# Optimization experiments

Measured on AMD Instinct MI355X. Metric: run time of the kernel, lower is better.

Reference implementation:

```python
import jax, jax.numpy as jnp
import numpy as np

N, E = 100000, 1600000
IN, EDGE_DIM, HID, OUT, HEADS = 128, 16, 32, 32, 2


def _glorot(key, shape, scale=0.1):
    return jax.random.normal(key, shape, dtype=jnp.float32) * scale


def setup_inputs() -> dict:
    key = jax.random.key(0)
    ks = jax.random.split(key, 20)
    HC1 = HEADS * HID
    return {
        "x": jax.random.normal(ks[0], (N, IN), dtype=jnp.float32),
        "edge_index": jax.random.randint(ks[1], (2, E), 0, N, dtype=jnp.int32),
        "edge_attr": jax.random.normal(ks[2], (E, EDGE_DIM), dtype=jnp.float32),
        # layer 1 (heads=HEADS, concat=True)
        "W1l": _glorot(ks[3], (IN, HC1)), "b1l": jnp.zeros((HC1,), jnp.float32),
        "W1r": _glorot(ks[4], (IN, HC1)), "b1r": jnp.zeros((HC1,), jnp.float32),
        "W1e": _glorot(ks[5], (EDGE_DIM, HC1)),
        "att1": _glorot(ks[6], (HEADS, HID)),
        "bias1": jnp.zeros((HC1,), jnp.float32),
        # layer 2 (heads=1, concat=False)
        "W2l": _glorot(ks[7], (HC1, HID)), "b2l": jnp.zeros((HID,), jnp.float32),
        "W2r": _glorot(ks[8], (HC1, HID)), "b2r": jnp.zeros((HID,), jnp.float32),
        "W2e": _glorot(ks[9], (EDGE_DIM, HID)),
        "att2": _glorot(ks[10], (1, HID)),
        "bias2": jnp.zeros((HID,), jnp.float32),
        # final linear
        "Wlin": _glorot(ks[11], (HID, OUT)), "blin": jnp.zeros((OUT,), jnp.float32),
    }


def gatv2_layer(x, src, dst, edge_attr, Wl, bl, Wr, br, We, att, bias, H, C, concat):
    n = x.shape[0]
    xl = (x @ Wl + bl).reshape(n, H, C)   # source transform (lin_l)
    xr = (x @ Wr + br).reshape(n, H, C)   # target transform (lin_r)
    ea = (edge_attr @ We).reshape(-1, H, C)
    m = xl[src] + xr[dst] + ea                       # [E, H, C]
    e = jnp.sum(jax.nn.leaky_relu(m, 0.2) * att, axis=-1)  # [E, H]
    # segment softmax over incoming edges of each destination node
    emax = jax.ops.segment_max(e, dst, num_segments=n)
    emax = jnp.where(jnp.isfinite(emax), emax, 0.0)
    ee = jnp.exp(e - emax[dst])
    denom = jax.ops.segment_sum(ee, dst, num_segments=n)
    alpha = ee / (denom[dst] + 1e-16)                # [E, H]
    out = jax.ops.segment_sum(xl[src] * alpha[..., None], dst, num_segments=n)  # [N, H, C]
    out = out.reshape(n, H * C) if concat else out.mean(axis=1)
    return out + bias


def reference(x, edge_index, edge_attr, W1l, b1l, W1r, b1r, W1e, att1, bias1,
              W2l, b2l, W2r, b2r, W2e, att2, bias2, Wlin, blin):
    src, dst = edge_index[0], edge_index[1]
    h = jax.nn.elu(gatv2_layer(x, src, dst, edge_attr, W1l, b1l, W1r, b1r, W1e,
                               att1, bias1, HEADS, HID, True))
    h = jax.nn.elu(gatv2_layer(h, src, dst, edge_attr, W2l, b2l, W2r, b2r, W2e,
                               att2, bias2, 1, HID, False))
    return h @ Wlin + blin
```

## Files before the change

### kernel.cpp

```cpp
#include <hip/hip_runtime.h>
#include <hip/hip_fp16.h>
#include <cstdint>
#include <cstddef>


typedef _Float16 half8 __attribute__((ext_vector_type(8)));
typedef float f32x4 __attribute__((ext_vector_type(4)));

__global__ void hist_kernel(const int* __restrict__ dst, int* __restrict__ deg, int E) {
    int e = blockIdx.x * blockDim.x + threadIdx.x;
    if (e < E) atomicAdd(&deg[dst[e]], 1);
}

__global__ void scan_part(const int* __restrict__ deg, int* __restrict__ bsum, int n) {
    int tid = threadIdx.x;
    int base = blockIdx.x * 1024 + tid * 4;
    int s = 0;
#pragma unroll
    for (int j = 0; j < 4; ++j) {
        int i = base + j;
        if (i < n) s += deg[i];
    }
#pragma unroll
    for (int off = 1; off < 64; off <<= 1) s += __shfl_xor(s, off, 64);
    __shared__ int ws[4];
    if ((tid & 63) == 0) ws[tid >> 6] = s;
    __syncthreads();
    if (tid == 0) bsum[blockIdx.x] = ws[0] + ws[1] + ws[2] + ws[3];
}

__global__ void scan_mid(int* __restrict__ bsum, int* __restrict__ rowstart, int nb, int n) {
    int tid = threadIdx.x;
    int v = (tid < nb) ? bsum[tid] : 0;
    int incl = v;
#pragma unroll
    for (int off = 1; off < 64; off <<= 1) {
        int t = __shfl_up(incl, off, 64);
        if ((tid & 63) >= off) incl += t;
    }
    __shared__ int w0;
    if (tid == 63) w0 = incl;
    __syncthreads();
    if (tid >= 64) incl += w0;
    if (tid < nb) bsum[tid] = incl - v;
    if (tid == nb - 1) rowstart[n] = incl;
}

__global__ void scan_fin(const int* __restrict__ deg, const int* __restrict__ bsum,
                         int* __restrict__ rowstart, int n) {
    int tid = threadIdx.x;
    int lane = tid & 63, wid = tid >> 6;
    int base = blockIdx.x * 1024 + tid * 4;
    int v[4];
    int s = 0;
#pragma unroll
    for (int j = 0; j < 4; ++j) {
        int i = base + j;
        v[j] = (i < n) ? deg[i] : 0;
        s += v[j];
    }
    int incl = s;
#pragma unroll
    for (int off = 1; off < 64; off <<= 1) {
        int t = __shfl_up(incl, off, 64);
        if (lane >= off) incl += t;
    }
    __shared__ int ws[4];
    if (lane == 63) ws[wid] = incl;
    __syncthreads();
    int wofs = 0;
    for (int w2 = 0; w2 < wid; ++w2) wofs += ws[w2];
    int acc = bsum[blockIdx.x] + wofs + (incl - s);
#pragma unroll
    for (int j = 0; j < 4; ++j) {
        int i = base + j;
        if (i < n) rowstart[i] = acc;
        acc += v[j];
    }
}

__global__ void scatter_kernel(const int* __restrict__ src, const int* __restrict__ dst,
                               const float* __restrict__ eattr,
                               const int* __restrict__ rowstart, int* __restrict__ cursor,
                               int* __restrict__ src_sorted, __half* __restrict__ eah_sorted,
                               int E) {
    int e = blockIdx.x * blockDim.x + threadIdx.x;
    if (e < E) {
        int d = dst[e];
        int p = atomicAdd(&cursor[d], 1);
        int pos = rowstart[d] + p;
        src_sorted[pos] = src[e];
        const float4* s4 = (const float4*)&eattr[(size_t)e * 16];
        float4 a = s4[0], b = s4[1], c = s4[2], f = s4[3];
        __half2 h[8];
        h[0] = __float22half2_rn(make_float2(a.x, a.y));
        h[1] = __float22half2_rn(make_float2(a.z, a.w));
        h[2] = __float22half2_rn(make_float2(b.x, b.y));
        h[3] = __float22half2_rn(make_float2(b.z, b.w));
        h[4] = __float22half2_rn(make_float2(c.x, c.y));
        h[5] = __float22half2_rn(make_float2(c.z, c.w));
        h[6] = __float22half2_rn(make_float2(f.x, f.y));
        h[7] = __float22half2_rn(make_float2(f.z, f.w));
        int4* o = (int4*)&eah_sorted[(size_t)pos * 16];
        o[0] = *(int4*)&h[0];
        o[1] = *(int4*)&h[4];
    }
}

template <int K, int Mh>
__global__ void wprep_kernel(const float* __restrict__ Wl, const float* __restrict__ Wr,
                             __half* __restrict__ Wfrag) {
    constexpr int KS = K / 32;
    constexpr int BN = 2 * Mh;
    int i = blockIdx.x * blockDim.x + threadIdx.x;
    if (i >= K * BN) return;
    int j = i & 7;
    int lane = (i >> 3) & 63;
    int rest = i >> 9;
    int ks = rest % KS;
    int nt = rest / KS;
    int k = ks * 32 + ((lane >> 4) & 3) * 8 + j;
    int col = nt * 16 + (lane & 15);
    float v = (col < Mh) ? Wl[k * Mh + col] : Wr[k * Mh + (col - Mh)];
    Wfrag[i] = __float2half(v);
}

template <int K, int Mh, int BM>
__global__ __launch_bounds__(256) void gemm_mfma(
    const float* __restrict__ x, const __half* __restrict__ Wfrag,
    const float* __restrict__ bl, const float* __restrict__ br,
    __half* __restrict__ yl, __half* __restrict__ yr, int n) {
    constexpr int BN = 2 * Mh;
    constexpr int KS = K / 32;
    constexpr int NT = BN / 16;
    constexpr int RW = BM / 64;
    constexpr int LDP = K + 8;
    __shared__ __half xs[BM * LDP];
    int tid = threadIdx.x;
    int lane = tid & 63;
    int wave = tid >> 6;
    int node0 = blockIdx.x * BM;
    constexpr int ITER = (BM * K) / (256 * 4);
#pragma unroll
    for (int it = 0; it < ITER; ++it) {
        int base = (it * 256 + tid) * 4;
        int row = base / K, kk = base % K;
        float4 v = make_float4(0.f, 0.f, 0.f, 0.f);
        if (node0 + row < n) v = *(const float4*)&x[(size_t)(node0 + row) * K + kk];
        __half2* d = (__half2*)&xs[row * LDP + kk];
        d[0] = __float22half2_rn(make_float2(v.x, v.y));
        d[1] = __float22half2_rn(make_float2(v.z, v.w));
    }
    __syncthreads();
    f32x4 acc[RW][NT];
#pragma unroll
    for (int r = 0; r < RW; ++r)
#pragma unroll
        for (int t = 0; t < NT; ++t) {
            f32x4 z = {0.f, 0.f, 0.f, 0.f};
            acc[r][t] = z;
        }
    int r0 = lane & 15, kof = (lane >> 4) * 8;
#pragma unroll
    for (int ks = 0; ks < KS; ++ks) {
        half8 a[RW];
#pragma unroll
        for (int r = 0; r < RW; ++r) {
            int row = (wave * RW + r) * 16 + r0;
            a[r] = *reinterpret_cast<const half8*>(&xs[row * LDP + ks * 32 + kof]);
        }
#pragma unroll
        for (int t = 0; t < NT; ++t) {
            half8 b = *reinterpret_cast<const half8*>(&Wfrag[(((size_t)t * KS + ks) * 64 + lane) * 8]);
#pragma unroll
            for (int r = 0; r < RW; ++r)
                acc[r][t] = __builtin_amdgcn_mfma_f32_16x16x32_f16(a[r], b, acc[r][t], 0, 0, 0);
        }
    }
#pragma unroll
    for (int r = 0; r < RW; ++r) {
#pragma unroll
        for (int t = 0; t < NT; ++t) {
            int col = t * 16 + (lane & 15);
            float bv = (col < Mh) ? bl[col] : br[col - Mh];
#pragma unroll
            for (int q = 0; q < 4; ++q) {
                int node = node0 + (wave * RW + r) * 16 + (lane >> 4) * 4 + q;
                if (node < n) {
                    float v = acc[r][t][q] + bv;
                    if (col < Mh) yl[(size_t)node * Mh + col] = __float2half(v);
                    else          yr[(size_t)node * Mh + (col - Mh)] = __float2half(v);
                }
            }
        }
    }
}

template <int K, int M, int NPB>
__global__ void linear_kernel(const float* __restrict__ x, const float* __restrict__ W,
                              const float* __restrict__ b, float* __restrict__ y, int n) {
    __shared__ float sx[NPB * K];
    int tid = threadIdx.x;
    int node0 = blockIdx.x * NPB;
    for (int i = tid; i < NPB * K; i += NPB * M) {
        int nn = node0 + i / K;
        sx[i] = (nn < n) ? x[(size_t)nn * K + (i % K)] : 0.f;
    }
    __syncthreads();
    int ln = tid / M, m = tid % M;
    int node = node0 + ln;
    if (node >= n) return;
    float acc = b[m];
#pragma unroll
    for (int k = 0; k < K; ++k) acc = fmaf(sx[ln * K + k], W[k * M + m], acc);
    y[(size_t)node * M + m] = acc;
}

template <int H, int C>
__global__ __launch_bounds__(256) void fused_edge_agg(
    const int* __restrict__ rowstart, const int* __restrict__ src_sorted,
    const __half* __restrict__ eah_sorted,
    const float* __restrict__ We,
    const float* __restrict__ att,
    const __half* __restrict__ xl, const __half* __restrict__ xr,
    const float* __restrict__ bias, float* __restrict__ out, int n) {
    constexpr int HC = H * C;
    constexpr int LPN = HC / 2;
    constexpr int NPW = 64 / LPN;
    int gt = blockIdx.x * blockDim.x + threadIdx.x;
    int wave = gt >> 6;
    int lane = threadIdx.x & 63;
    int sub = lane / LPN;
    int j = lane % LPN;
    int ch0 = 2 * j;
    int node = wave * NPW + sub;
    if (node >= n) return;
    __half2 wh[16];
#pragma unroll
    for (int k = 0; k < 16; ++k) wh[k] = __float22half2_rn(*(const float2*)&We[k * HC + ch0]);
    float2 a2 = *(const float2*)&att[ch0];
    float2 xr2 = __half22float2(*(const __half2*)&xr[(size_t)node * HC + ch0]);
    int beg = rowstart[node], end = rowstart[node + 1];
    float denom = 0.f, acc0 = 0.f, acc1 = 0.f;

    auto gemv = [&](const float4& r0, const float4& r1, const __half2& xlh,
                    float& m0, float& m1, float2& xlf) {
        const __half2* h0 = (const __half2*)&r0;
        const __half2* h1 = (const __half2*)&r1;
        __half2 p0 = __hmul2(__low2half2(h0[0]), wh[0]);
        __half2 p1 = __hmul2(__high2half2(h0[0]), wh[1]);
        p0 = __hfma2(__low2half2(h0[1]), wh[2], p0);
        p1 = __hfma2(__high2half2(h0[1]), wh[3], p1);
        p0 = __hfma2(__low2half2(h0[2]), wh[4], p0);
        p1 = __hfma2(__high2half2(h0[2]), wh[5], p1);
        p0 = __hfma2(__low2half2(h0[3]), wh[6], p0);
        p1 = __hfma2(__high2half2(h0[3]), wh[7], p1);
        p0 = __hfma2(__low2half2(h1[0]), wh[8], p0);
        p1 = __hfma2(__high2half2(h1[0]), wh[9], p1);
        p0 = __hfma2(__low2half2(h1[1]), wh[10], p0);
        p1 = __hfma2(__high2half2(h1[1]), wh[11], p1);
        p0 = __hfma2(__low2half2(h1[2]), wh[12], p0);
        p1 = __hfma2(__high2half2(h1[2]), wh[13], p1);
        p0 = __hfma2(__low2half2(h1[3]), wh[14], p0);
        p1 = __hfma2(__high2half2(h1[3]), wh[15], p1);
        float2 mf = __half22float2(__hadd2(p0, p1));
        xlf = __half22float2(xlh);
        m0 = xlf.x + xr2.x + mf.x;
        m1 = xlf.y + xr2.y + mf.y;
    };
    auto logit = [&](float m0, float m1) -> float {
        m0 = (m0 > 0.f) ? m0 : 0.2f * m0;
        m1 = (m1 > 0.f) ? m1 : 0.2f * m1;
        float v = m0 * a2.x + m1 * a2.y;
#pragma unroll
        for (int msk = 1; msk < 16; msk <<= 1) v += __shfl_xor(v, msk, 64);
        return v;
    };

    int pp = beg;
    for (; pp + 2 <= end; pp += 2) {
        int s0 = src_sorted[pp];
        int s1 = src_sorted[pp + 1];
        const float4* qa = (const float4*)&eah_sorted[(size_t)pp * 16];
        const float4* qb = (const float4*)&eah_sorted[((size_t)pp + 1) * 16];
        float4 r0a = qa[0], r1a = qa[1];
        float4 r0b = qb[0], r1b = qb[1];
        __half2 xh0 = *(const __half2*)&xl[(size_t)s0 * HC + ch0];
        __half2 xh1 = *(const __half2*)&xl[(size_t)s1 * HC + ch0];
        float m0a, m1a, m0b, m1b;
        float2 xla, xlb;
        gemv(r0a, r1a, xh0, m0a, m1a, xla);
        gemv(r0b, r1b, xh1, m0b, m1b, xlb);
        float wa = __expf(logit(m0a, m1a));
        float wb = __expf(logit(m0b, m1b));
        denom += wa + wb;
        acc0 = fmaf(xla.x, wa, acc0);
        acc1 = fmaf(xla.y, wa, acc1);
        acc0 = fmaf(xlb.x, wb, acc0);
        acc1 = fmaf(xlb.y, wb, acc1);
    }
    if (pp < end) {
        int s0 = src_sorted[pp];
        const float4* qa = (const float4*)&eah_sorted[(size_t)pp * 16];
        float4 r0a = qa[0], r1a = qa[1];
        __half2 xh0 = *(const __half2*)&xl[(size_t)s0 * HC + ch0];
        float m0a, m1a;
        float2 xla;
        gemv(r0a, r1a, xh0, m0a, m1a, xla);
        float wa = __expf(logit(m0a, m1a));
        denom += wa;
        acc0 = fmaf(xla.x, wa, acc0);
        acc1 = fmaf(xla.y, wa, acc1);
    }
    float2 b2 = *(const float2*)&bias[ch0];
    float inv = 1.f / (denom + 1e-16f);
    float o0 = acc0 * inv + b2.x;
    float o1 = acc1 * inv + b2.y;
    o0 = (o0 > 0.f) ? o0 : __expf(o0) - 1.f;
    o1 = (o1 > 0.f) ? o1 : __expf(o1) - 1.f;
    *(float2*)&out[(size_t)node * HC + ch0] = make_float2(o0, o1);
}

extern "C" void kernel_launch(void* const* d_in, const int* in_sizes, int n_in,
                              void* d_out, int out_size, void* d_ws, size_t ws_size,
                              hipStream_t stream) {
    const float* x     = (const float*)d_in[0];
    const int*   eidx  = (const int*)d_in[1];
    const float* eattr = (const float*)d_in[2];
    const float* W1l   = (const float*)d_in[3];
    const float* b1l   = (const float*)d_in[4];
    const float* W1r   = (const float*)d_in[5];
    const float* b1r   = (const float*)d_in[6];
    const float* W1e   = (const float*)d_in[7];
    const float* att1  = (const float*)d_in[8];
    const float* bias1 = (const float*)d_in[9];
    const float* W2l   = (const float*)d_in[10];
    const float* b2l   = (const float*)d_in[11];
    const float* W2r   = (const float*)d_in[12];
    const float* b2r   = (const float*)d_in[13];
    const float* W2e   = (const float*)d_in[14];
    const float* att2  = (const float*)d_in[15];
    const float* bias2 = (const float*)d_in[16];
    const float* Wlin  = (const float*)d_in[17];
    const float* blin  = (const float*)d_in[18];

    const int N = in_sizes[0] / 128;
    const int E = in_sizes[1] / 2;
    const int* src = eidx;
    const int* dst = eidx + E;

    char* p = (char*)d_ws;
    auto take = [&](size_t bytes) {
        char* r = p;
        p += (bytes + 255) & ~(size_t)255;
        return r;
    };
    int*    deg        = (int*)take((size_t)N * sizeof(int));
    int*    cursor     = (int*)take((size_t)N * sizeof(int));
    int*    rowstart   = (int*)take((size_t)(N + 1) * sizeof(int));
    int*    bsum       = (int*)take(256 * sizeof(int));
    int*    src_sorted = (int*)take((size_t)E * sizeof(int));
    __half* eah_sorted = (__half*)take((size_t)E * 16 * sizeof(__half));
    __half* A          = (__half*)take((size_t)N * 64 * sizeof(__half));
    __half* B          = (__half*)take((size_t)N * 64 * sizeof(__half));
    float*  Cbuf       = (float*)take((size_t)N * 64 * sizeof(float));
    __half* Wf1        = (__half*)take((size_t)128 * 128 * sizeof(__half));
    __half* Wf2        = (__half*)take((size_t)64 * 64 * sizeof(__half));

    (void)hipMemsetAsync(deg, 0, (size_t)N * sizeof(int), stream);
    (void)hipMemsetAsync(cursor, 0, (size_t)N * sizeof(int), stream);
    hist_kernel<<<(E + 255) / 256, 256, 0, stream>>>(dst, deg, E);
    {
        int nb = (N + 1023) / 1024;
        scan_part<<<nb, 256, 0, stream>>>(deg, bsum, N);
        scan_mid<<<1, 128, 0, stream>>>(bsum, rowstart, nb, N);
        scan_fin<<<nb, 256, 0, stream>>>(deg, bsum, rowstart, N);
    }
    scatter_kernel<<<(E + 255) / 256, 256, 0, stream>>>(src, dst, eattr, rowstart, cursor,
                                                        src_sorted, eah_sorted, E);
    wprep_kernel<128, 64><<<(128 * 128 + 255) / 256, 256, 0, stream>>>(W1l, W1r, Wf1);
    wprep_kernel<64, 32><<<(64 * 64 + 255) / 256, 256, 0, stream>>>(W2l, W2r, Wf2);

    gemm_mfma<128, 64, 64><<<(N + 63) / 64, 256, 0, stream>>>(x, Wf1, b1l, b1r, A, B, N);
    fused_edge_agg<2, 32><<<(int)(((size_t)((N + 1) / 2) * 64 + 255) / 256), 256, 0, stream>>>(
        rowstart, src_sorted, eah_sorted, W1e, att1, A, B, bias1, Cbuf, N);

    gemm_mfma<64, 32, 128><<<(N + 127) / 128, 256, 0, stream>>>(Cbuf, Wf2, b2l, b2r, A, B, N);
    fused_edge_agg<1, 32><<<(int)(((size_t)((N + 3) / 4) * 64 + 255) / 256), 256, 0, stream>>>(
        rowstart, src_sorted, eah_sorted, W2e, att2, A, B, bias2, Cbuf, N);

    linear_kernel<32, 32, 8><<<(N + 7) / 8, 256, 0, stream>>>(Cbuf, Wlin, blin, (float*)d_out, N);
}
```

Baseline: 457.9 us.

## Sort nodes by degree and keep edge attributes in original order

Adds a degree-bucketed node permutation so each wave processes nodes of similar in-degree, which reduces intra-wave divergence in the edge loop. The scatter now writes fp16 edge attributes in original edge order with coalesced stores, and stores (edge id, src) pairs in CSR order. The aggregation kernel reads attributes indirectly through that edge id. This turns the gather of edge attributes into random 32-byte reads and adds three small preprocessing kernels. It also merges the two memsets into one.

```diff
diff --git a/kernel.cpp b/kernel.cpp
--- a/kernel.cpp
+++ b/kernel.cpp
@@ -82,14 +82,12 @@
 __global__ void scatter_kernel(const int* __restrict__ src, const int* __restrict__ dst,
                                const float* __restrict__ eattr,
                                const int* __restrict__ rowstart, int* __restrict__ cursor,
-                               int* __restrict__ src_sorted, __half* __restrict__ eah_sorted,
-                               int E) {
+                               int2* __restrict__ es, __half* __restrict__ eah, int E) {
     int e = blockIdx.x * blockDim.x + threadIdx.x;
     if (e < E) {
         int d = dst[e];
         int p = atomicAdd(&cursor[d], 1);
-        int pos = rowstart[d] + p;
-        src_sorted[pos] = src[e];
+        es[rowstart[d] + p] = make_int2(e, src[e]);
         const float4* s4 = (const float4*)&eattr[(size_t)e * 16];
         float4 a = s4[0], b = s4[1], c = s4[2], f = s4[3];
         __half2 h[8];
@@ -101,9 +99,52 @@
         h[5] = __float22half2_rn(make_float2(c.z, c.w));
         h[6] = __float22half2_rn(make_float2(f.x, f.y));
         h[7] = __float22half2_rn(make_float2(f.z, f.w));
-        int4* o = (int4*)&eah_sorted[(size_t)pos * 16];
+        int4* o = (int4*)&eah[(size_t)e * 16];
         o[0] = *(int4*)&h[0];
         o[1] = *(int4*)&h[4];
+    }
+}
+
+__global__ void dhist_kernel(const int* __restrict__ deg, int* __restrict__ dcount, int n) {
+    int i = blockIdx.x * blockDim.x + threadIdx.x;
+    if (i < n) {
+        int b = deg[i];
+        b = (b > 255) ? 255 : b;
+        atomicAdd(&dcount[b], 1);
+    }
+}
+
+__global__ void dscan_kernel(const int* __restrict__ dcount, int* __restrict__ dstart) {
+    int tid = threadIdx.x;
+    int v[4];
+    int s = 0;
+#pragma unroll
+    for (int j = 0; j < 4; ++j) {
+        v[j] = dcount[tid * 4 + j];
+        s += v[j];
+    }
+    int incl = s;
+#pragma unroll
+    for (int off = 1; off < 64; off <<= 1) {
+        int t = __shfl_up(incl, off, 64);
+        if (tid >= off) incl += t;
+    }
+    int acc = incl - s;
+#pragma unroll
+    for (int j = 0; j < 4; ++j) {
+        dstart[tid * 4 + j] = acc;
+        acc += v[j];
+    }
+}
+
+__global__ void dscatter_kernel(const int* __restrict__ deg, const int* __restrict__ dstart,
+                                int* __restrict__ dcur, int* __restrict__ nodeperm, int n) {
+    int i = blockIdx.x * blockDim.x + threadIdx.x;
+    if (i < n) {
+        int b = deg[i];
+        b = (b > 255) ? 255 : b;
+        int p = atomicAdd(&dcur[b], 1);
+        nodeperm[dstart[b] + p] = i;
     }
 }
 
@@ -218,8 +259,8 @@
 
 template <int H, int C>
 __global__ __launch_bounds__(256) void fused_edge_agg(
-    const int* __restrict__ rowstart, const int* __restrict__ src_sorted,
-    const __half* __restrict__ eah_sorted,
+    const int* __restrict__ rowstart, const int2* __restrict__ es,
+    const __half* __restrict__ eah, const int* __restrict__ nodeperm,
     const float* __restrict__ We,
     const float* __restrict__ att,
     const __half* __restrict__ xl, const __half* __restrict__ xr,
@@ -233,8 +274,9 @@
     int sub = lane / LPN;
     int j = lane % LPN;
     int ch0 = 2 * j;
-    int node = wave * NPW + sub;
-    if (node >= n) return;
+    int slot = wave * NPW + sub;
+    if (slot >= n) return;
+    int node = nodeperm[slot];
     __half2 wh[16];
 #pragma unroll
     for (int k = 0; k < 16; ++k) wh[k] = __float22half2_rn(*(const float2*)&We[k * HC + ch0]);
@@ -279,14 +321,14 @@
 
     int pp = beg;
     for (; pp + 2 <= end; pp += 2) {
-        int s0 = src_sorted[pp];
-        int s1 = src_sorted[pp + 1];
-        const float4* qa = (const float4*)&eah_sorted[(size_t)pp * 16];
-        const float4* qb = (const float4*)&eah_sorted[((size_t)pp + 1) * 16];
+        int2 ea = es[pp];
+        int2 eb = es[pp + 1];
+        const float4* qa = (const float4*)&eah[(size_t)ea.x * 16];
+        const float4* qb = (const float4*)&eah[(size_t)eb.x * 16];
         float4 r0a = qa[0], r1a = qa[1];
         float4 r0b = qb[0], r1b = qb[1];
-        __half2 xh0 = *(const __half2*)&xl[(size_t)s0 * HC + ch0];
-        __half2 xh1 = *(const __half2*)&xl[(size_t)s1 * HC + ch0];
+        __half2 xh0 = *(const __half2*)&xl[(size_t)ea.y * HC + ch0];
+        __half2 xh1 = *(const __half2*)&xl[(size_t)eb.y * HC + ch0];
         float m0a, m1a, m0b, m1b;
         float2 xla, xlb;
         gemv(r0a, r1a, xh0, m0a, m1a, xla);
@@ -300,10 +342,10 @@
         acc1 = fmaf(xlb.y, wb, acc1);
     }
     if (pp < end) {
-        int s0 = src_sorted[pp];
-        const float4* qa = (const float4*)&eah_sorted[(size_t)pp * 16];
+        int2 ea = es[pp];
+        const float4* qa = (const float4*)&eah[(size_t)ea.x * 16];
         float4 r0a = qa[0], r1a = qa[1];
-        __half2 xh0 = *(const __half2*)&xl[(size_t)s0 * HC + ch0];
+        __half2 xh0 = *(const __half2*)&xl[(size_t)ea.y * HC + ch0];
         float m0a, m1a;
         float2 xla;
         gemv(r0a, r1a, xh0, m0a, m1a, xla);
@@ -355,20 +397,24 @@
         p += (bytes + 255) & ~(size_t)255;
         return r;
     };
-    int*    deg        = (int*)take((size_t)N * sizeof(int));
-    int*    cursor     = (int*)take((size_t)N * sizeof(int));
-    int*    rowstart   = (int*)take((size_t)(N + 1) * sizeof(int));
-    int*    bsum       = (int*)take(256 * sizeof(int));
-    int*    src_sorted = (int*)take((size_t)E * sizeof(int));
-    __half* eah_sorted = (__half*)take((size_t)E * 16 * sizeof(__half));
-    __half* A          = (__half*)take((size_t)N * 64 * sizeof(__half));
-    __half* B          = (__half*)take((size_t)N * 64 * sizeof(__half));
-    float*  Cbuf       = (float*)take((size_t)N * 64 * sizeof(float));
-    __half* Wf1        = (__half*)take((size_t)128 * 128 * sizeof(__half));
-    __half* Wf2        = (__half*)take((size_t)64 * 64 * sizeof(__half));
-
-    (void)hipMemsetAsync(deg, 0, (size_t)N * sizeof(int), stream);
-    (void)hipMemsetAsync(cursor, 0, (size_t)N * sizeof(int), stream);
+    int*    deg      = (int*)take((size_t)N * sizeof(int));
+    int*    cursor   = (int*)take((size_t)N * sizeof(int));
+    int*    dcount   = (int*)take(256 * sizeof(int));
+    int*    dcur     = (int*)take(256 * sizeof(int));
+    char*   zero_end = p;
+    int*    rowstart = (int*)take((size_t)(N + 1) * sizeof(int));
+    int*    bsum     = (int*)take(256 * sizeof(int));
+    int*    dstart   = (int*)take(256 * sizeof(int));
+    int*    nodeperm = (int*)take((size_t)N * sizeof(int));
+    int2*   es       = (int2*)take((size_t)E * sizeof(int2));
+    __half* eah      = (__half*)take((size_t)E * 16 * sizeof(__half));
+    __half* A        = (__half*)take((size_t)N * 64 * sizeof(__half));
+    __half* B        = (__half*)take((size_t)N * 64 * sizeof(__half));
+    float*  Cbuf     = (float*)take((size_t)N * 64 * sizeof(float));
+    __half* Wf1      = (__half*)take((size_t)128 * 128 * sizeof(__half));
+    __half* Wf2      = (__half*)take((size_t)64 * 64 * sizeof(__half));
+
+    (void)hipMemsetAsync(deg, 0, (size_t)(zero_end - (char*)deg), stream);
     hist_kernel<<<(E + 255) / 256, 256, 0, stream>>>(dst, deg, E);
     {
         int nb = (N + 1023) / 1024;
@@ -376,18 +422,27 @@
         scan_mid<<<1, 128, 0, stream>>>(bsum, rowstart, nb, N);
         scan_fin<<<nb, 256, 0, stream>>>(deg, bsum, rowstart, N);
     }
-    scatter_kernel<<<(E + 255) / 256, 256, 0, stream>>>(src, dst, eattr, rowstart, cursor,
-                                                        src_sorted, eah_sorted, E);
+    scatter_kernel<<<(E + 255) / 256, 256, 0, stream>>>(src, dst, eattr, rowstart, cursor, es,
+                                                        eah, E);
+    dhist_kernel<<<(N + 255) / 256, 256, 0, stream>>>(deg, dcount, N);
+    dscan_kernel<<<1, 64, 0, stream>>>(dcount, dstart);
+    dscatter_kernel<<<(N + 255) / 256, 256, 0, stream>>>(deg, dstart, dcur, nodeperm, N);
     wprep_kernel<128, 64><<<(128 * 128 + 255) / 256, 256, 0, stream>>>(W1l, W1r, Wf1);
     wprep_kernel<64, 32><<<(64 * 64 + 255) / 256, 256, 0, stream>>>(W2l, W2r, Wf2);
 
     gemm_mfma<128, 64, 64><<<(N + 63) / 64, 256, 0, stream>>>(x, Wf1, b1l, b1r, A, B, N);
-    fused_edge_agg<2, 32><<<(int)(((size_t)((N + 1) / 2) * 64 + 255) / 256), 256, 0, stream>>>(
-        rowstart, src_sorted, eah_sorted, W1e, att1, A, B, bias1, Cbuf, N);
+    {
+        long waves = (N + 1) / 2;
+        fused_edge_agg<2, 32><<<(int)((waves * 64 + 255) / 256), 256, 0, stream>>>(
+            rowstart, es, eah, nodeperm, W1e, att1, A, B, bias1, Cbuf, N);
+    }
 
     gemm_mfma<64, 32, 128><<<(N + 127) / 128, 256, 0, stream>>>(Cbuf, Wf2, b2l, b2r, A, B, N);
-    fused_edge_agg<1, 32><<<(int)(((size_t)((N + 3) / 4) * 64 + 255) / 256), 256, 0, stream>>>(
-        rowstart, src_sorted, eah_sorted, W2e, att2, A, B, bias2, Cbuf, N);
+    {
+        long waves = (N + 3) / 4;
+        fused_edge_agg<1, 32><<<(int)((waves * 64 + 255) / 256), 256, 0, stream>>>(
+            rowstart, es, eah, nodeperm, W2e, att2, A, B, bias2, Cbuf, N);
+    }
 
     linear_kernel<32, 32, 8><<<(N + 7) / 8, 256, 0, stream>>>(Cbuf, Wlin, blin, (float*)d_out, N);
 }
```

After: 934.7 us. 2.04x slower.
